# Kernel optimization log

Measured on AMD Instinct MI355X. Metric: run time of the kernel, lower is better.

The kernel has to match this reference:

```python
import jax, jax.numpy as jnp
import numpy as np

INPUT_SIZE, HIDDEN, OUTPUT = 6, 64, 3
B, T = 4096, 512


def setup_inputs() -> dict:
    key = jax.random.key(0)
    ks = jax.random.split(key, 12)
    s = 1.0 / np.sqrt(HIDDEN)  # torch LSTM/Linear default init scale
    u = lambda k, shape: jax.random.uniform(k, shape, jnp.float32, -s, s)
    return {
        "x": jax.random.normal(ks[0], (B, T, INPUT_SIZE), jnp.float32),
        "Wih0": u(ks[1], (4 * HIDDEN, INPUT_SIZE)),
        "Whh0": u(ks[2], (4 * HIDDEN, HIDDEN)),
        "bih0": u(ks[3], (4 * HIDDEN,)),
        "bhh0": u(ks[4], (4 * HIDDEN,)),
        "Wih1": u(ks[5], (4 * HIDDEN, HIDDEN)),
        "Whh1": u(ks[6], (4 * HIDDEN, HIDDEN)),
        "bih1": u(ks[7], (4 * HIDDEN,)),
        "bhh1": u(ks[8], (4 * HIDDEN,)),
        "Wfc": u(ks[9], (OUTPUT, HIDDEN)),
        "bfc": u(ks[10], (OUTPUT,)),
    }


def _lstm_layer(x, Wih, Whh, bih, bhh):
    # x: [B, T, F] -> hidden sequence [B, T, H]; torch gate order i,f,g,o
    Bn = x.shape[0]
    H = Whh.shape[1]
    b = bih + bhh
    # precompute input projections for all steps: [T, B, 4H]
    gx = jnp.einsum('btf,gf->tbg', x, Wih) + b

    def step(carry, gxt):
        h, c = carry
        gates = gxt + h @ Whh.T
        i, f, g, o = jnp.split(gates, 4, axis=-1)
        i, f, o = jax.nn.sigmoid(i), jax.nn.sigmoid(f), jax.nn.sigmoid(o)
        g = jnp.tanh(g)
        c = f * c + i * g
        h = o * jnp.tanh(c)
        return (h, c), h

    h0 = jnp.zeros((Bn, H), x.dtype)
    c0 = jnp.zeros((Bn, H), x.dtype)
    (_, _), hs = jax.lax.scan(step, (h0, c0), gx)  # hs: [T, B, H]
    return hs.transpose(1, 0, 2)


def reference(x, Wih0, Whh0, bih0, bhh0, Wih1, Whh1, bih1, bhh1, Wfc, bfc):
    h1 = _lstm_layer(x, Wih0, Whh0, bih0, bhh0)
    h2 = _lstm_layer(h1, Wih1, Whh1, bih1, bhh1)
    last = h2[:, -1, :]              # [B, H]
    return last @ Wfc.T + bfc        # [B, OUTPUT]
```

## Files before the change

kernel.cpp:

```cpp
#include <hip/hip_runtime.h>

#define H    64
#define TT   512
#define NB   16
#define OUTD 3
#define BTOT 4096
#define INF  6

typedef _Float16 f16;
typedef _Float16 f16x8 __attribute__((ext_vector_type(8)));
typedef float    f32x4 __attribute__((ext_vector_type(4)));
typedef float    f32x2 __attribute__((ext_vector_type(2)));

#define AS 168

#define LOG2E 1.44269504088896340736f
#define KSC   (2.0f * LOG2E)

static __device__ __forceinline__ f32x2 pk_fma(f32x2 a, f32x2 b, f32x2 c) {
#if __has_builtin(__builtin_elementwise_fma)
    return __builtin_elementwise_fma(a, b, c);
#else
    f32x2 r; r.x = __builtin_fmaf(a.x, b.x, c.x); r.y = __builtin_fmaf(a.y, b.y, c.y);
    return r;
#endif
}

__device__ __forceinline__ f32x2 lstm_cell2(f32x2 ai, f32x2 af, f32x2 ag, f32x2 ao,
                                            f32x2& C) {
    f32x2 ei, ef, eg, eo;
    ei.x = __builtin_amdgcn_exp2f(ai.x); ei.y = __builtin_amdgcn_exp2f(ai.y);
    ef.x = __builtin_amdgcn_exp2f(af.x); ef.y = __builtin_amdgcn_exp2f(af.y);
    eg.x = __builtin_amdgcn_exp2f(ag.x); eg.y = __builtin_amdgcn_exp2f(ag.y);
    eo.x = __builtin_amdgcn_exp2f(ao.x); eo.y = __builtin_amdgcn_exp2f(ao.y);
    f32x2 A  = ei + 1.0f;
    f32x2 F  = ef + 1.0f;
    f32x2 Bp = eg + 1.0f;
    f32x2 G  = eg - 1.0f;
    f32x2 P  = A * Bp;
    f32x2 PF = P * F;
    f32x2 r1; r1.x = __builtin_amdgcn_rcpf(PF.x); r1.y = __builtin_amdgcn_rcpf(PF.y);
    f32x2 n1 = ef * C * P;
    f32x2 t2 = ei * G * F;
    f32x2 k2 = {KSC, KSC};
    C = pk_fma(k2, t2, n1) * r1;
    f32x2 Cc; Cc.x = fminf(C.x, 126.0f); Cc.y = fminf(C.y, 126.0f);
    f32x2 ec; ec.x = __builtin_amdgcn_exp2f(Cc.x); ec.y = __builtin_amdgcn_exp2f(Cc.y);
    f32x2 D2 = (eo + 1.0f) * (ec + 1.0f);
    f32x2 r2; r2.x = __builtin_amdgcn_rcpf(D2.x); r2.y = __builtin_amdgcn_rcpf(D2.y);
    return eo * (ec - 1.0f) * r2;
}

__launch_bounds__(512, 2)
__global__ void lstm_ws(const float* __restrict__ x,
                        const float* __restrict__ Wih0, const float* __restrict__ Whh0,
                        const float* __restrict__ bih0, const float* __restrict__ bhh0,
                        const float* __restrict__ Wih1, const float* __restrict__ Whh1,
                        const float* __restrict__ bih1, const float* __restrict__ bhh1,
                        const float* __restrict__ Wfc,  const float* __restrict__ bfc,
                        float* __restrict__ out)
{
    __shared__ __align__(16) f16 Phi[2][NB * AS];
    __shared__ float hfin[NB][H + 1];

    const int t    = threadIdx.x;
    const int u    = t & 255;
    const int role = t >> 8;
    const int wv   = u >> 6;
    const int l15  = u & 15;
    const int q    = (u >> 4) & 3;
    const int jj   = 16 * wv + l15;
    const int b0   = blockIdx.x * NB;
    const int ar   = l15 * AS;
    const int ko   = q * 8;

    {
        f16* ph = &Phi[0][0];
        for (int idx = t; idx < 2 * NB * AS; idx += 512) ph[idx] = (f16)0.0f;
    }
    __syncthreads();

    const bool loader = (role == 0) && (u < NB * INF);
    const int  xb = u / INF;
    const int  xf = u - xb * INF;
    if (loader)
        Phi[0][xb * AS + 128 + xf] = (f16)x[((size_t)(b0 + xb) * TT) * INF + xf];
    __syncthreads();

    if (role == 0) {
        f16x8 wh0[2][4];
        f16x8 wx0[4];
        f32x4 bC0[4];
        #pragma unroll
        for (int g = 0; g < 4; ++g) {
            const float sc = (g == 2) ? (2.0f * LOG2E) : LOG2E;
            const int n = 64 * g + jj;
            #pragma unroll
            for (int kt = 0; kt < 2; ++kt) {
                f16x8 v;
                #pragma unroll
                for (int j = 0; j < 8; ++j)
                    v[j] = (f16)(Whh0[n * H + kt * 32 + q * 8 + j] * sc);
                wh0[kt][g] = v;
            }
            f16x8 vx;
            #pragma unroll
            for (int j = 0; j < 8; ++j)
                vx[j] = (q == 0 && j < INF) ? (f16)(Wih0[n * INF + j] * sc) : (f16)0.0f;
            wx0[g] = vx;
            const float bu = (bih0[64 * g + jj] + bhh0[64 * g + jj]) * sc;
            bC0[g] = (f32x4){bu, bu, bu, bu};
        }
        f32x2 c01 = {0.f, 0.f}, c23 = {0.f, 0.f};
        float xpre = 0.0f;

        auto stepL0 = [&](f16* __restrict__ AH, f16* __restrict__ BH, int s) {
            if (loader) {
                const int tn = (s + 1 < TT) ? (s + 1) : (TT - 1);
                xpre = x[((size_t)(b0 + xb) * TT + tn) * INF + xf];
            }
            f16x8 a0 = *(const f16x8*)&AH[ar + 0   + ko];
            f16x8 a1 = *(const f16x8*)&AH[ar + 32  + ko];
            f16x8 ax = *(const f16x8*)&BH[ar + 128 + ko];
            f32x4 accA[4];
            #pragma unroll
            for (int g = 0; g < 4; ++g) {
                f32x4 acc;
                acc = __builtin_amdgcn_mfma_f32_16x16x32_f16(a0, wh0[0][g], bC0[g], 0, 0, 0);
                acc = __builtin_amdgcn_mfma_f32_16x16x32_f16(a1, wh0[1][g], acc, 0, 0, 0);
                acc = __builtin_amdgcn_mfma_f32_16x16x32_f16(ax, wx0[g],    acc, 0, 0, 0);
                accA[g] = acc;
            }
            f32x2 h01 = lstm_cell2((f32x2){accA[0][0], accA[0][1]},
                                   (f32x2){accA[1][0], accA[1][1]},
                                   (f32x2){accA[2][0], accA[2][1]},
                                   (f32x2){accA[3][0], accA[3][1]}, c01);
            f32x2 h23 = lstm_cell2((f32x2){accA[0][2], accA[0][3]},
                                   (f32x2){accA[1][2], accA[1][3]},
                                   (f32x2){accA[2][2], accA[2][3]},
                                   (f32x2){accA[3][2], accA[3][3]}, c23);
            BH[(q * 4 + 0) * AS + jj] = (f16)h01.x;
            BH[(q * 4 + 1) * AS + jj] = (f16)h01.y;
            BH[(q * 4 + 2) * AS + jj] = (f16)h23.x;
            BH[(q * 4 + 3) * AS + jj] = (f16)h23.y;
            if (loader) AH[xb * AS + 128 + xf] = (f16)xpre;
            __syncthreads();
        };

        for (int s = 0; s < TT; s += 2) {
            stepL0(Phi[1], Phi[0], s);
            stepL0(Phi[0], Phi[1], s + 1);
        }
        __syncthreads();
    } else {
        f16x8 wi1[2][4];
        f16x8 wh1[2][4];
        f32x4 bC1[4];
        #pragma unroll
        for (int g = 0; g < 4; ++g) {
            const float sc = (g == 2) ? (2.0f * LOG2E) : LOG2E;
            const int n = 64 * g + jj;
            #pragma unroll
            for (int kt = 0; kt < 2; ++kt) {
                f16x8 v1, v2;
                #pragma unroll
                for (int j = 0; j < 8; ++j) {
                    const int k = kt * 32 + q * 8 + j;
                    v1[j] = (f16)(Wih1[n * H + k] * sc);
                    v2[j] = (f16)(Whh1[n * H + k] * sc);
                }
                wi1[kt][g] = v1; wh1[kt][g] = v2;
            }
            const float bu = (bih1[64 * g + jj] + bhh1[64 * g + jj]) * sc;
            bC1[g] = (f32x4){bu, bu, bu, bu};
        }
        f32x2 c01 = {0.f, 0.f}, c23 = {0.f, 0.f};

        __syncthreads();

        auto stepL1 = [&](f16* __restrict__ AH, f16* __restrict__ BH, int s) {
            f16x8 n0 = *(const f16x8*)&AH[ar + 0  + ko];
            f16x8 n1 = *(const f16x8*)&AH[ar + 32 + ko];
            f16x8 r0 = *(const f16x8*)&BH[ar + 64 + ko];
            f16x8 r1 = *(const f16x8*)&BH[ar + 96 + ko];
            f32x4 accB[4];
            #pragma unroll
            for (int g = 0; g < 4; ++g) {
                f32x4 acc;
                acc = __builtin_amdgcn_mfma_f32_16x16x32_f16(n0, wi1[0][g], bC1[g], 0, 0, 0);
                acc = __builtin_amdgcn_mfma_f32_16x16x32_f16(n1, wi1[1][g], acc, 0, 0, 0);
                acc = __builtin_amdgcn_mfma_f32_16x16x32_f16(r0, wh1[0][g], acc, 0, 0, 0);
                acc = __builtin_amdgcn_mfma_f32_16x16x32_f16(r1, wh1[1][g], acc, 0, 0, 0);
                accB[g] = acc;
            }
            f32x2 h01 = lstm_cell2((f32x2){accB[0][0], accB[0][1]},
                                   (f32x2){accB[1][0], accB[1][1]},
                                   (f32x2){accB[2][0], accB[2][1]},
                                   (f32x2){accB[3][0], accB[3][1]}, c01);
            f32x2 h23 = lstm_cell2((f32x2){accB[0][2], accB[0][3]},
                                   (f32x2){accB[1][2], accB[1][3]},
                                   (f32x2){accB[2][2], accB[2][3]},
                                   (f32x2){accB[3][2], accB[3][3]}, c23);
            AH[(q * 4 + 0) * AS + 64 + jj] = (f16)h01.x;
            AH[(q * 4 + 1) * AS + 64 + jj] = (f16)h01.y;
            AH[(q * 4 + 2) * AS + 64 + jj] = (f16)h23.x;
            AH[(q * 4 + 3) * AS + 64 + jj] = (f16)h23.y;
            if (s == TT) {
                hfin[q * 4 + 0][jj] = h01.x;
                hfin[q * 4 + 1][jj] = h01.y;
                hfin[q * 4 + 2][jj] = h23.x;
                hfin[q * 4 + 3][jj] = h23.y;
            }
            __syncthreads();
        };

        for (int s = 1; s <= TT; s += 2) {
            stepL1(Phi[0], Phi[1], s);
            stepL1(Phi[1], Phi[0], s + 1);
        }
    }

    if (t < NB * OUTD) {
        const int b = t / OUTD;
        const int o = t - b * OUTD;
        float a = bfc[o];
        #pragma unroll
        for (int j = 0; j < H; ++j)
            a += Wfc[o * H + j] * hfin[b][j];
        out[(size_t)(b0 + b) * OUTD + o] = a;
    }
}

extern "C" void kernel_launch(void* const* d_in, const int* in_sizes, int n_in,
                              void* d_out, int out_size, void* d_ws, size_t ws_size,
                              hipStream_t stream) {
    const float* x    = (const float*)d_in[0];
    const float* Wih0 = (const float*)d_in[1];
    const float* Whh0 = (const float*)d_in[2];
    const float* bih0 = (const float*)d_in[3];
    const float* bhh0 = (const float*)d_in[4];
    const float* Wih1 = (const float*)d_in[5];
    const float* Whh1 = (const float*)d_in[6];
    const float* bih1 = (const float*)d_in[7];
    const float* bhh1 = (const float*)d_in[8];
    const float* Wfc  = (const float*)d_in[9];
    const float* bfc  = (const float*)d_in[10];

    dim3 grid(BTOT / NB);
    dim3 block(512);
    lstm_ws<<<grid, block, 0, stream>>>(x, Wih0, Whh0, bih0, bhh0,
                                        Wih1, Whh1, bih1, bhh1,
                                        Wfc, bfc, (float*)d_out);
}
```

Before: 415.7 us.

## Duplicate each LSTM role across two wave groups and split cell math between them

```diff
diff --git a/kernel.cpp b/kernel.cpp
--- a/kernel.cpp
+++ b/kernel.cpp
@@ -22,6 +22,15 @@
     return __builtin_elementwise_fma(a, b, c);
 #else
     f32x2 r; r.x = __builtin_fmaf(a.x, b.x, c.x); r.y = __builtin_fmaf(a.y, b.y, c.y);
+    return r;
+#endif
+}
+
+static __device__ __forceinline__ f32x2 pk_min(f32x2 a, f32x2 b) {
+#if __has_builtin(__builtin_elementwise_min)
+    return __builtin_elementwise_min(a, b);
+#else
+    f32x2 r; r.x = fminf(a.x, b.x); r.y = fminf(a.y, b.y);
     return r;
 #endif
 }
@@ -44,14 +53,15 @@
     f32x2 t2 = ei * G * F;
     f32x2 k2 = {KSC, KSC};
     C = pk_fma(k2, t2, n1) * r1;
-    f32x2 Cc; Cc.x = fminf(C.x, 126.0f); Cc.y = fminf(C.y, 126.0f);
+    f32x2 clim = {126.0f, 126.0f};
+    f32x2 Cc = pk_min(C, clim);
     f32x2 ec; ec.x = __builtin_amdgcn_exp2f(Cc.x); ec.y = __builtin_amdgcn_exp2f(Cc.y);
     f32x2 D2 = (eo + 1.0f) * (ec + 1.0f);
     f32x2 r2; r2.x = __builtin_amdgcn_rcpf(D2.x); r2.y = __builtin_amdgcn_rcpf(D2.y);
     return eo * (ec - 1.0f) * r2;
 }
 
-__launch_bounds__(512, 2)
+__launch_bounds__(1024, 4)
 __global__ void lstm_ws(const float* __restrict__ x,
                         const float* __restrict__ Wih0, const float* __restrict__ Whh0,
                         const float* __restrict__ bih0, const float* __restrict__ bhh0,
@@ -65,7 +75,9 @@
 
     const int t    = threadIdx.x;
     const int u    = t & 255;
-    const int role = t >> 8;
+    const int pair = (t >> 8) & 3;
+    const int role = pair & 1;
+    const int rr   = pair >> 1;
     const int wv   = u >> 6;
     const int l15  = u & 15;
     const int q    = (u >> 4) & 3;
@@ -76,11 +88,11 @@
 
     {
         f16* ph = &Phi[0][0];
-        for (int idx = t; idx < 2 * NB * AS; idx += 512) ph[idx] = (f16)0.0f;
+        for (int idx = t; idx < 2 * NB * AS; idx += 1024) ph[idx] = (f16)0.0f;
     }
     __syncthreads();
 
-    const bool loader = (role == 0) && (u < NB * INF);
+    const bool loader = (pair == 0) && (u < NB * INF);
     const int  xb = u / INF;
     const int  xf = u - xb * INF;
     if (loader)
@@ -111,7 +123,7 @@
             const float bu = (bih0[64 * g + jj] + bhh0[64 * g + jj]) * sc;
             bC0[g] = (f32x4){bu, bu, bu, bu};
         }
-        f32x2 c01 = {0.f, 0.f}, c23 = {0.f, 0.f};
+        f32x2 c2 = {0.f, 0.f};
         float xpre = 0.0f;
 
         auto stepL0 = [&](f16* __restrict__ AH, f16* __restrict__ BH, int s) {
@@ -131,18 +143,21 @@
                 acc = __builtin_amdgcn_mfma_f32_16x16x32_f16(ax, wx0[g],    acc, 0, 0, 0);
                 accA[g] = acc;
             }
-            f32x2 h01 = lstm_cell2((f32x2){accA[0][0], accA[0][1]},
-                                   (f32x2){accA[1][0], accA[1][1]},
-                                   (f32x2){accA[2][0], accA[2][1]},
-                                   (f32x2){accA[3][0], accA[3][1]}, c01);
-            f32x2 h23 = lstm_cell2((f32x2){accA[0][2], accA[0][3]},
-                                   (f32x2){accA[1][2], accA[1][3]},
-                                   (f32x2){accA[2][2], accA[2][3]},
-                                   (f32x2){accA[3][2], accA[3][3]}, c23);
-            BH[(q * 4 + 0) * AS + jj] = (f16)h01.x;
-            BH[(q * 4 + 1) * AS + jj] = (f16)h01.y;
-            BH[(q * 4 + 2) * AS + jj] = (f16)h23.x;
-            BH[(q * 4 + 3) * AS + jj] = (f16)h23.y;
+            if (rr == 0) {
+                f32x2 hv = lstm_cell2((f32x2){accA[0][0], accA[0][1]},
+                                      (f32x2){accA[1][0], accA[1][1]},
+                                      (f32x2){accA[2][0], accA[2][1]},
+                                      (f32x2){accA[3][0], accA[3][1]}, c2);
+                BH[(q * 4 + 0) * AS + jj] = (f16)hv.x;
+                BH[(q * 4 + 1) * AS + jj] = (f16)hv.y;
+            } else {
+                f32x2 hv = lstm_cell2((f32x2){accA[0][2], accA[0][3]},
+                                      (f32x2){accA[1][2], accA[1][3]},
+                                      (f32x2){accA[2][2], accA[2][3]},
+                                      (f32x2){accA[3][2], accA[3][3]}, c2);
+                BH[(q * 4 + 2) * AS + jj] = (f16)hv.x;
+                BH[(q * 4 + 3) * AS + jj] = (f16)hv.y;
+            }
             if (loader) AH[xb * AS + 128 + xf] = (f16)xpre;
             __syncthreads();
         };
@@ -174,7 +189,7 @@
             const float bu = (bih1[64 * g + jj] + bhh1[64 * g + jj]) * sc;
             bC1[g] = (f32x4){bu, bu, bu, bu};
         }
-        f32x2 c01 = {0.f, 0.f}, c23 = {0.f, 0.f};
+        f32x2 c2 = {0.f, 0.f};
 
         __syncthreads();
 
@@ -193,23 +208,28 @@
                 acc = __builtin_amdgcn_mfma_f32_16x16x32_f16(r1, wh1[1][g], acc, 0, 0, 0);
                 accB[g] = acc;
             }
-            f32x2 h01 = lstm_cell2((f32x2){accB[0][0], accB[0][1]},
-                                   (f32x2){accB[1][0], accB[1][1]},
-                                   (f32x2){accB[2][0], accB[2][1]},
-                                   (f32x2){accB[3][0], accB[3][1]}, c01);
-            f32x2 h23 = lstm_cell2((f32x2){accB[0][2], accB[0][3]},
-                                   (f32x2){accB[1][2], accB[1][3]},
-                                   (f32x2){accB[2][2], accB[2][3]},
-                                   (f32x2){accB[3][2], accB[3][3]}, c23);
-            AH[(q * 4 + 0) * AS + 64 + jj] = (f16)h01.x;
-            AH[(q * 4 + 1) * AS + 64 + jj] = (f16)h01.y;
-            AH[(q * 4 + 2) * AS + 64 + jj] = (f16)h23.x;
-            AH[(q * 4 + 3) * AS + 64 + jj] = (f16)h23.y;
-            if (s == TT) {
-                hfin[q * 4 + 0][jj] = h01.x;
-                hfin[q * 4 + 1][jj] = h01.y;
-                hfin[q * 4 + 2][jj] = h23.x;
-                hfin[q * 4 + 3][jj] = h23.y;
+            if (rr == 0) {
+                f32x2 hv = lstm_cell2((f32x2){accB[0][0], accB[0][1]},
+                                      (f32x2){accB[1][0], accB[1][1]},
+                                      (f32x2){accB[2][0], accB[2][1]},
+                                      (f32x2){accB[3][0], accB[3][1]}, c2);
+                AH[(q * 4 + 0) * AS + 64 + jj] = (f16)hv.x;
+                AH[(q * 4 + 1) * AS + 64 + jj] = (f16)hv.y;
+                if (s == TT) {
+                    hfin[q * 4 + 0][jj] = hv.x;
+                    hfin[q * 4 + 1][jj] = hv.y;
+                }
+            } else {
+                f32x2 hv = lstm_cell2((f32x2){accB[0][2], accB[0][3]},
+                                      (f32x2){accB[1][2], accB[1][3]},
+                                      (f32x2){accB[2][2], accB[2][3]},
+                                      (f32x2){accB[3][2], accB[3][3]}, c2);
+                AH[(q * 4 + 2) * AS + 64 + jj] = (f16)hv.x;
+                AH[(q * 4 + 3) * AS + 64 + jj] = (f16)hv.y;
+                if (s == TT) {
+                    hfin[q * 4 + 2][jj] = hv.x;
+                    hfin[q * 4 + 3][jj] = hv.y;
+                }
             }
             __syncthreads();
         };
@@ -247,7 +267,7 @@
     const float* bfc  = (const float*)d_in[10];
 
     dim3 grid(BTOT / NB);
-    dim3 block(512);
+    dim3 block(1024);
     lstm_ws<<<grid, block, 0, stream>>>(x, Wih0, Whh0, bih0, bhh0,
                                         Wih1, Whh1, bih1, bhh1,
                                         Wfc, bfc, (float*)d_out);
```

Measured after the change: 519.7 us. +25.0%, slower.

## Replace block barriers with LDS flag counters and 4-deep ring buffers between layers

Applied to the files above, without the earlier changes.

```diff
diff --git a/kernel.cpp b/kernel.cpp
--- a/kernel.cpp
+++ b/kernel.cpp
@@ -6,13 +6,14 @@
 #define OUTD 3
 #define BTOT 4096
 #define INF  6
+#define RD   4
+#define HS   72
+#define XS   32
 
 typedef _Float16 f16;
 typedef _Float16 f16x8 __attribute__((ext_vector_type(8)));
 typedef float    f32x4 __attribute__((ext_vector_type(4)));
 typedef float    f32x2 __attribute__((ext_vector_type(2)));
-
-#define AS 168
 
 #define LOG2E 1.44269504088896340736f
 #define KSC   (2.0f * LOG2E)
@@ -22,6 +23,15 @@
     return __builtin_elementwise_fma(a, b, c);
 #else
     f32x2 r; r.x = __builtin_fmaf(a.x, b.x, c.x); r.y = __builtin_fmaf(a.y, b.y, c.y);
+    return r;
+#endif
+}
+
+static __device__ __forceinline__ f32x2 pk_min(f32x2 a, f32x2 b) {
+#if __has_builtin(__builtin_elementwise_min)
+    return __builtin_elementwise_min(a, b);
+#else
+    f32x2 r; r.x = fminf(a.x, b.x); r.y = fminf(a.y, b.y);
     return r;
 #endif
 }
@@ -44,11 +54,23 @@
     f32x2 t2 = ei * G * F;
     f32x2 k2 = {KSC, KSC};
     C = pk_fma(k2, t2, n1) * r1;
-    f32x2 Cc; Cc.x = fminf(C.x, 126.0f); Cc.y = fminf(C.y, 126.0f);
+    f32x2 clim = {126.0f, 126.0f};
+    f32x2 Cc = pk_min(C, clim);
     f32x2 ec; ec.x = __builtin_amdgcn_exp2f(Cc.x); ec.y = __builtin_amdgcn_exp2f(Cc.y);
     f32x2 D2 = (eo + 1.0f) * (ec + 1.0f);
     f32x2 r2; r2.x = __builtin_amdgcn_rcpf(D2.x); r2.y = __builtin_amdgcn_rcpf(D2.y);
     return eo * (ec - 1.0f) * r2;
+}
+
+static __device__ __forceinline__ void wait_ge(const unsigned* p, unsigned tgt) {
+    volatile const unsigned* vp = (volatile const unsigned*)p;
+    while (*vp < tgt) {}
+    asm volatile("" ::: "memory");
+}
+
+static __device__ __forceinline__ void bump(unsigned* p, bool lane0) {
+    asm volatile("s_waitcnt lgkmcnt(0)" ::: "memory");
+    if (lane0) atomicAdd(p, 1u);
 }
 
 __launch_bounds__(512, 2)
@@ -60,31 +82,35 @@
                         const float* __restrict__ Wfc,  const float* __restrict__ bfc,
                         float* __restrict__ out)
 {
-    __shared__ __align__(16) f16 Phi[2][NB * AS];
+    __shared__ __align__(16) f16 H0r[RD][NB * HS];
+    __shared__ __align__(16) f16 H1r[RD][NB * HS];
+    __shared__ __align__(16) f16 Xr[RD][NB * XS];
     __shared__ float hfin[NB][H + 1];
-
-    const int t    = threadIdx.x;
-    const int u    = t & 255;
-    const int role = t >> 8;
-    const int wv   = u >> 6;
-    const int l15  = u & 15;
-    const int q    = (u >> 4) & 3;
-    const int jj   = 16 * wv + l15;
-    const int b0   = blockIdx.x * NB;
-    const int ar   = l15 * AS;
-    const int ko   = q * 8;
-
-    {
-        f16* ph = &Phi[0][0];
-        for (int idx = t; idx < 2 * NB * AS; idx += 512) ph[idx] = (f16)0.0f;
-    }
+    __shared__ unsigned flg[12];
+
+    const int t     = threadIdx.x;
+    const int u     = t & 255;
+    const int role  = t >> 8;
+    const int wv    = u >> 6;
+    const int l15   = u & 15;
+    const int q     = (u >> 4) & 3;
+    const int jj    = 16 * wv + l15;
+    const int b0    = blockIdx.x * NB;
+    const int ar    = l15 * HS;
+    const int ko    = q * 8;
+    const bool lane0 = (t & 63) == 0;
+
+    for (int idx = t; idx < RD * NB * HS; idx += 512) (&H0r[0][0])[idx] = (f16)0.0f;
+    for (int idx = t; idx < RD * NB * HS; idx += 512) (&H1r[0][0])[idx] = (f16)0.0f;
+    for (int idx = t; idx < RD * NB * XS; idx += 512) (&Xr[0][0])[idx]  = (f16)0.0f;
+    if (t < 12) flg[t] = 0u;
     __syncthreads();
 
     const bool loader = (role == 0) && (u < NB * INF);
     const int  xb = u / INF;
     const int  xf = u - xb * INF;
     if (loader)
-        Phi[0][xb * AS + 128 + xf] = (f16)x[((size_t)(b0 + xb) * TT) * INF + xf];
+        Xr[0][xb * XS + xf] = (f16)x[((size_t)(b0 + xb) * TT) * INF + xf];
     __syncthreads();
 
     if (role == 0) {
@@ -114,14 +140,20 @@
         f32x2 c01 = {0.f, 0.f}, c23 = {0.f, 0.f};
         float xpre = 0.0f;
 
-        auto stepL0 = [&](f16* __restrict__ AH, f16* __restrict__ BH, int s) {
+        #pragma unroll 4
+        for (int s = 0; s < TT; ++s) {
+            const int j  = s & 3;
+            const int jp = (s - 1) & 3;
+            const int jn = (s + 1) & 3;
+            if (s > 0) wait_ge(&flg[jp], 4u * (unsigned)((s - 1) >> 2) + 4u);
             if (loader) {
                 const int tn = (s + 1 < TT) ? (s + 1) : (TT - 1);
                 xpre = x[((size_t)(b0 + xb) * TT + tn) * INF + xf];
             }
-            f16x8 a0 = *(const f16x8*)&AH[ar + 0   + ko];
-            f16x8 a1 = *(const f16x8*)&AH[ar + 32  + ko];
-            f16x8 ax = *(const f16x8*)&BH[ar + 128 + ko];
+            const f16* Ah = &H0r[jp][0];
+            f16x8 a0 = *(const f16x8*)&Ah[ar + 0  + ko];
+            f16x8 a1 = *(const f16x8*)&Ah[ar + 32 + ko];
+            f16x8 ax = *(const f16x8*)&Xr[j][l15 * XS + ko];
             f32x4 accA[4];
             #pragma unroll
             for (int g = 0; g < 4; ++g) {
@@ -139,19 +171,15 @@
                                    (f32x2){accA[1][2], accA[1][3]},
                                    (f32x2){accA[2][2], accA[2][3]},
                                    (f32x2){accA[3][2], accA[3][3]}, c23);
-            BH[(q * 4 + 0) * AS + jj] = (f16)h01.x;
-            BH[(q * 4 + 1) * AS + jj] = (f16)h01.y;
-            BH[(q * 4 + 2) * AS + jj] = (f16)h23.x;
-            BH[(q * 4 + 3) * AS + jj] = (f16)h23.y;
-            if (loader) AH[xb * AS + 128 + xf] = (f16)xpre;
-            __syncthreads();
-        };
-
-        for (int s = 0; s < TT; s += 2) {
-            stepL0(Phi[1], Phi[0], s);
-            stepL0(Phi[0], Phi[1], s + 1);
-        }
-        __syncthreads();
+            if (s >= RD) wait_ge(&flg[8 + j], 4u * (unsigned)(s >> 2));
+            f16* Bh = &H0r[j][0];
+            Bh[(q * 4 + 0) * HS + jj] = (f16)h01.x;
+            Bh[(q * 4 + 1) * HS + jj] = (f16)h01.y;
+            Bh[(q * 4 + 2) * HS + jj] = (f16)h23.x;
+            Bh[(q * 4 + 3) * HS + jj] = (f16)h23.y;
+            if (loader) Xr[jn][xb * XS + xf] = (f16)xpre;
+            bump(&flg[j], lane0);
+        }
     } else {
         f16x8 wi1[2][4];
         f16x8 wh1[2][4];
@@ -176,13 +204,19 @@
         }
         f32x2 c01 = {0.f, 0.f}, c23 = {0.f, 0.f};
 
-        __syncthreads();
-
-        auto stepL1 = [&](f16* __restrict__ AH, f16* __restrict__ BH, int s) {
-            f16x8 n0 = *(const f16x8*)&AH[ar + 0  + ko];
-            f16x8 n1 = *(const f16x8*)&AH[ar + 32 + ko];
-            f16x8 r0 = *(const f16x8*)&BH[ar + 64 + ko];
-            f16x8 r1 = *(const f16x8*)&BH[ar + 96 + ko];
+        #pragma unroll 4
+        for (int m = 0; m < TT; ++m) {
+            const int j  = m & 3;
+            const int jp = (m - 1) & 3;
+            wait_ge(&flg[j], 4u * (unsigned)(m >> 2) + 4u);
+            if (m > 0) wait_ge(&flg[4 + jp], 4u * (unsigned)((m - 1) >> 2) + 4u);
+            const f16* Nh = &H0r[j][0];
+            const f16* Rh = &H1r[jp][0];
+            f16x8 n0 = *(const f16x8*)&Nh[ar + 0  + ko];
+            f16x8 n1 = *(const f16x8*)&Nh[ar + 32 + ko];
+            f16x8 r0 = *(const f16x8*)&Rh[ar + 0  + ko];
+            f16x8 r1 = *(const f16x8*)&Rh[ar + 32 + ko];
+            bump(&flg[8 + j], lane0);
             f32x4 accB[4];
             #pragma unroll
             for (int g = 0; g < 4; ++g) {
@@ -199,26 +233,24 @@
                                    (f32x2){accB[3][0], accB[3][1]}, c01);
             f32x2 h23 = lstm_cell2((f32x2){accB[0][2], accB[0][3]},
                                    (f32x2){accB[1][2], accB[1][3]},
-                                   (f32x2){accB[2][2], accB[2][3]},
+                                   (f32x2){accB[2][2], accB[2][3]}, 
                                    (f32x2){accB[3][2], accB[3][3]}, c23);
-            AH[(q * 4 + 0) * AS + 64 + jj] = (f16)h01.x;
-            AH[(q * 4 + 1) * AS + 64 + jj] = (f16)h01.y;
-            AH[(q * 4 + 2) * AS + 64 + jj] = (f16)h23.x;
-            AH[(q * 4 + 3) * AS + 64 + jj] = (f16)h23.y;
-            if (s == TT) {
+            f16* Wh = &H1r[j][0];
+            Wh[(q * 4 + 0) * HS + jj] = (f16)h01.x;
+            Wh[(q * 4 + 1) * HS + jj] = (f16)h01.y;
+            Wh[(q * 4 + 2) * HS + jj] = (f16)h23.x;
+            Wh[(q * 4 + 3) * HS + jj] = (f16)h23.y;
+            if (m == TT - 1) {
                 hfin[q * 4 + 0][jj] = h01.x;
                 hfin[q * 4 + 1][jj] = h01.y;
                 hfin[q * 4 + 2][jj] = h23.x;
                 hfin[q * 4 + 3][jj] = h23.y;
             }
-            __syncthreads();
-        };
-
-        for (int s = 1; s <= TT; s += 2) {
-            stepL1(Phi[0], Phi[1], s);
-            stepL1(Phi[1], Phi[0], s + 1);
+            bump(&flg[4 + j], lane0);
         }
     }
+
+    __syncthreads();
 
     if (t < NB * OUTD) {
         const int b = t / OUTD;
```

Measured after the change: 494.8 us. 1.19x slower.

## Fuse both LSTM layers into a single 256-thread wavefront schedule per block

Applied to the files above, without the earlier changes.

```diff
diff --git a/kernel.cpp b/kernel.cpp
--- a/kernel.cpp
+++ b/kernel.cpp
@@ -6,13 +6,13 @@
 #define OUTD 3
 #define BTOT 4096
 #define INF  6
+#define HS   72
+#define XS   32
 
 typedef _Float16 f16;
 typedef _Float16 f16x8 __attribute__((ext_vector_type(8)));
 typedef float    f32x4 __attribute__((ext_vector_type(4)));
 typedef float    f32x2 __attribute__((ext_vector_type(2)));
-
-#define AS 168
 
 #define LOG2E 1.44269504088896340736f
 #define KSC   (2.0f * LOG2E)
@@ -22,6 +22,15 @@
     return __builtin_elementwise_fma(a, b, c);
 #else
     f32x2 r; r.x = __builtin_fmaf(a.x, b.x, c.x); r.y = __builtin_fmaf(a.y, b.y, c.y);
+    return r;
+#endif
+}
+
+static __device__ __forceinline__ f32x2 pk_min(f32x2 a, f32x2 b) {
+#if __has_builtin(__builtin_elementwise_min)
+    return __builtin_elementwise_min(a, b);
+#else
+    f32x2 r; r.x = fminf(a.x, b.x); r.y = fminf(a.y, b.y);
     return r;
 #endif
 }
@@ -44,180 +53,175 @@
     f32x2 t2 = ei * G * F;
     f32x2 k2 = {KSC, KSC};
     C = pk_fma(k2, t2, n1) * r1;
-    f32x2 Cc; Cc.x = fminf(C.x, 126.0f); Cc.y = fminf(C.y, 126.0f);
+    f32x2 clim = {126.0f, 126.0f};
+    f32x2 Cc = pk_min(C, clim);
     f32x2 ec; ec.x = __builtin_amdgcn_exp2f(Cc.x); ec.y = __builtin_amdgcn_exp2f(Cc.y);
     f32x2 D2 = (eo + 1.0f) * (ec + 1.0f);
     f32x2 r2; r2.x = __builtin_amdgcn_rcpf(D2.x); r2.y = __builtin_amdgcn_rcpf(D2.y);
     return eo * (ec - 1.0f) * r2;
 }
 
-__launch_bounds__(512, 2)
-__global__ void lstm_ws(const float* __restrict__ x,
-                        const float* __restrict__ Wih0, const float* __restrict__ Whh0,
-                        const float* __restrict__ bih0, const float* __restrict__ bhh0,
-                        const float* __restrict__ Wih1, const float* __restrict__ Whh1,
-                        const float* __restrict__ bih1, const float* __restrict__ bhh1,
-                        const float* __restrict__ Wfc,  const float* __restrict__ bfc,
-                        float* __restrict__ out)
+__launch_bounds__(256, 1)
+__global__ void lstm_fused(const float* __restrict__ x,
+                           const float* __restrict__ Wih0, const float* __restrict__ Whh0,
+                           const float* __restrict__ bih0, const float* __restrict__ bhh0,
+                           const float* __restrict__ Wih1, const float* __restrict__ Whh1,
+                           const float* __restrict__ bih1, const float* __restrict__ bhh1,
+                           const float* __restrict__ Wfc,  const float* __restrict__ bfc,
+                           float* __restrict__ out)
 {
-    __shared__ __align__(16) f16 Phi[2][NB * AS];
+    __shared__ __align__(16) f16 H0[2][NB * HS];
+    __shared__ __align__(16) f16 H1[2][NB * HS];
+    __shared__ __align__(16) f16 Xr[2][NB * XS];
     __shared__ float hfin[NB][H + 1];
 
-    const int t    = threadIdx.x;
-    const int u    = t & 255;
-    const int role = t >> 8;
-    const int wv   = u >> 6;
-    const int l15  = u & 15;
-    const int q    = (u >> 4) & 3;
-    const int jj   = 16 * wv + l15;
-    const int b0   = blockIdx.x * NB;
-    const int ar   = l15 * AS;
-    const int ko   = q * 8;
+    const int t   = threadIdx.x;
+    const int wv  = t >> 6;
+    const int l15 = t & 15;
+    const int q   = (t >> 4) & 3;
+    const int jj  = 16 * wv + l15;
+    const int b0  = blockIdx.x * NB;
+    const int ar  = l15 * HS;
+    const int ko  = q * 8;
+
+    for (int idx = t; idx < 2 * NB * HS; idx += 256) {
+        (&H0[0][0])[idx] = (f16)0.0f;
+        (&H1[0][0])[idx] = (f16)0.0f;
+    }
+    for (int idx = t; idx < 2 * NB * XS; idx += 256) (&Xr[0][0])[idx] = (f16)0.0f;
+    __syncthreads();
+
+    const bool loader = t < NB * INF;
+    const int  xb = t / INF;
+    const int  xf = t - xb * INF;
+    if (loader)
+        Xr[0][xb * XS + xf] = (f16)x[((size_t)(b0 + xb) * TT) * INF + xf];
+
+    f16x8 wh0[2][4], wx0[4], wi1[2][4], wh1[2][4];
+    f32x4 bC0[4], bC1[4];
+    #pragma unroll
+    for (int g = 0; g < 4; ++g) {
+        const float sc = (g == 2) ? KSC : LOG2E;
+        const int n = 64 * g + jj;
+        #pragma unroll
+        for (int kt = 0; kt < 2; ++kt) {
+            f16x8 v0, v1, v2;
+            #pragma unroll
+            for (int j = 0; j < 8; ++j) {
+                const int k = kt * 32 + q * 8 + j;
+                v0[j] = (f16)(Whh0[n * H + k] * sc);
+                v1[j] = (f16)(Wih1[n * H + k] * sc);
+                v2[j] = (f16)(Whh1[n * H + k] * sc);
+            }
+            wh0[kt][g] = v0; wi1[kt][g] = v1; wh1[kt][g] = v2;
+        }
+        f16x8 vx;
+        #pragma unroll
+        for (int j = 0; j < 8; ++j)
+            vx[j] = (q == 0 && j < INF) ? (f16)(Wih0[n * INF + j] * sc) : (f16)0.0f;
+        wx0[g] = vx;
+        const float bu0 = (bih0[64 * g + jj] + bhh0[64 * g + jj]) * sc;
+        const float bu1 = (bih1[64 * g + jj] + bhh1[64 * g + jj]) * sc;
+        bC0[g] = (f32x4){bu0, bu0, bu0, bu0};
+        bC1[g] = (f32x4){bu1, bu1, bu1, bu1};
+    }
+    f32x2 c0a = {0.f, 0.f}, c0b = {0.f, 0.f};
+    f32x2 c1a = {0.f, 0.f}, c1b = {0.f, 0.f};
+    float xpre = 0.0f;
+    __syncthreads();
+
+    auto mfmaA = [&](f16x8 a0, f16x8 a1, f16x8 ax, f32x4* acc) {
+        #pragma unroll
+        for (int g = 0; g < 4; ++g) {
+            f32x4 a = __builtin_amdgcn_mfma_f32_16x16x32_f16(a0, wh0[0][g], bC0[g], 0, 0, 0);
+            a = __builtin_amdgcn_mfma_f32_16x16x32_f16(a1, wh0[1][g], a, 0, 0, 0);
+            a = __builtin_amdgcn_mfma_f32_16x16x32_f16(ax, wx0[g],    a, 0, 0, 0);
+            acc[g] = a;
+        }
+    };
+    auto mfmaB = [&](f16x8 a0, f16x8 a1, f16x8 r0, f16x8 r1, f32x4* acc) {
+        #pragma unroll
+        for (int g = 0; g < 4; ++g) {
+            f32x4 a = __builtin_amdgcn_mfma_f32_16x16x32_f16(a0, wi1[0][g], bC1[g], 0, 0, 0);
+            a = __builtin_amdgcn_mfma_f32_16x16x32_f16(a1, wi1[1][g], a, 0, 0, 0);
+            a = __builtin_amdgcn_mfma_f32_16x16x32_f16(r0, wh1[0][g], a, 0, 0, 0);
+            a = __builtin_amdgcn_mfma_f32_16x16x32_f16(r1, wh1[1][g], a, 0, 0, 0);
+            acc[g] = a;
+        }
+    };
+    auto cellWrite = [&](f32x4* acc, f32x2& ca, f32x2& cb, f16* dst) {
+        f32x2 h01 = lstm_cell2((f32x2){acc[0][0], acc[0][1]},
+                               (f32x2){acc[1][0], acc[1][1]},
+                               (f32x2){acc[2][0], acc[2][1]},
+                               (f32x2){acc[3][0], acc[3][1]}, ca);
+        f32x2 h23 = lstm_cell2((f32x2){acc[0][2], acc[0][3]},
+                               (f32x2){acc[1][2], acc[1][3]},
+                               (f32x2){acc[2][2], acc[2][3]}, 
+                               (f32x2){acc[3][2], acc[3][3]}, cb);
+        dst[(q * 4 + 0) * HS + jj] = (f16)h01.x;
+        dst[(q * 4 + 1) * HS + jj] = (f16)h01.y;
+        dst[(q * 4 + 2) * HS + jj] = (f16)h23.x;
+        dst[(q * 4 + 3) * HS + jj] = (f16)h23.y;
+    };
 
     {
-        f16* ph = &Phi[0][0];
-        for (int idx = t; idx < 2 * NB * AS; idx += 512) ph[idx] = (f16)0.0f;
-    }
-    __syncthreads();
-
-    const bool loader = (role == 0) && (u < NB * INF);
-    const int  xb = u / INF;
-    const int  xf = u - xb * INF;
-    if (loader)
-        Phi[0][xb * AS + 128 + xf] = (f16)x[((size_t)(b0 + xb) * TT) * INF + xf];
-    __syncthreads();
-
-    if (role == 0) {
-        f16x8 wh0[2][4];
-        f16x8 wx0[4];
-        f32x4 bC0[4];
-        #pragma unroll
-        for (int g = 0; g < 4; ++g) {
-            const float sc = (g == 2) ? (2.0f * LOG2E) : LOG2E;
-            const int n = 64 * g + jj;
-            #pragma unroll
-            for (int kt = 0; kt < 2; ++kt) {
-                f16x8 v;
-                #pragma unroll
-                for (int j = 0; j < 8; ++j)
-                    v[j] = (f16)(Whh0[n * H + kt * 32 + q * 8 + j] * sc);
-                wh0[kt][g] = v;
-            }
-            f16x8 vx;
-            #pragma unroll
-            for (int j = 0; j < 8; ++j)
-                vx[j] = (q == 0 && j < INF) ? (f16)(Wih0[n * INF + j] * sc) : (f16)0.0f;
-            wx0[g] = vx;
-            const float bu = (bih0[64 * g + jj] + bhh0[64 * g + jj]) * sc;
-            bC0[g] = (f32x4){bu, bu, bu, bu};
-        }
-        f32x2 c01 = {0.f, 0.f}, c23 = {0.f, 0.f};
-        float xpre = 0.0f;
-
-        auto stepL0 = [&](f16* __restrict__ AH, f16* __restrict__ BH, int s) {
-            if (loader) {
-                const int tn = (s + 1 < TT) ? (s + 1) : (TT - 1);
-                xpre = x[((size_t)(b0 + xb) * TT + tn) * INF + xf];
-            }
-            f16x8 a0 = *(const f16x8*)&AH[ar + 0   + ko];
-            f16x8 a1 = *(const f16x8*)&AH[ar + 32  + ko];
-            f16x8 ax = *(const f16x8*)&BH[ar + 128 + ko];
-            f32x4 accA[4];
-            #pragma unroll
-            for (int g = 0; g < 4; ++g) {
-                f32x4 acc;
-                acc = __builtin_amdgcn_mfma_f32_16x16x32_f16(a0, wh0[0][g], bC0[g], 0, 0, 0);
-                acc = __builtin_amdgcn_mfma_f32_16x16x32_f16(a1, wh0[1][g], acc, 0, 0, 0);
-                acc = __builtin_amdgcn_mfma_f32_16x16x32_f16(ax, wx0[g],    acc, 0, 0, 0);
-                accA[g] = acc;
-            }
-            f32x2 h01 = lstm_cell2((f32x2){accA[0][0], accA[0][1]},
-                                   (f32x2){accA[1][0], accA[1][1]},
-                                   (f32x2){accA[2][0], accA[2][1]},
-                                   (f32x2){accA[3][0], accA[3][1]}, c01);
-            f32x2 h23 = lstm_cell2((f32x2){accA[0][2], accA[0][3]},
-                                   (f32x2){accA[1][2], accA[1][3]},
-                                   (f32x2){accA[2][2], accA[2][3]},
-                                   (f32x2){accA[3][2], accA[3][3]}, c23);
-            BH[(q * 4 + 0) * AS + jj] = (f16)h01.x;
-            BH[(q * 4 + 1) * AS + jj] = (f16)h01.y;
-            BH[(q * 4 + 2) * AS + jj] = (f16)h23.x;
-            BH[(q * 4 + 3) * AS + jj] = (f16)h23.y;
-            if (loader) AH[xb * AS + 128 + xf] = (f16)xpre;
-            __syncthreads();
-        };
-
-        for (int s = 0; s < TT; s += 2) {
-            stepL0(Phi[1], Phi[0], s);
-            stepL0(Phi[0], Phi[1], s + 1);
-        }
+        if (loader) xpre = x[((size_t)(b0 + xb) * TT + 1) * INF + xf];
+        const f16* h0r = &H0[1][0];
+        f16x8 a0 = *(const f16x8*)&h0r[ar + ko];
+        f16x8 a1 = *(const f16x8*)&h0r[ar + 32 + ko];
+        f16x8 ax = *(const f16x8*)&Xr[0][l15 * XS + ko];
+        f32x4 accA[4];
+        mfmaA(a0, a1, ax, accA);
+        cellWrite(accA, c0a, c0b, &H0[0][0]);
+        if (loader) Xr[1][xb * XS + xf] = (f16)xpre;
         __syncthreads();
-    } else {
-        f16x8 wi1[2][4];
-        f16x8 wh1[2][4];
-        f32x4 bC1[4];
-        #pragma unroll
-        for (int g = 0; g < 4; ++g) {
-            const float sc = (g == 2) ? (2.0f * LOG2E) : LOG2E;
-            const int n = 64 * g + jj;
-            #pragma unroll
-            for (int kt = 0; kt < 2; ++kt) {
-                f16x8 v1, v2;
-                #pragma unroll
-                for (int j = 0; j < 8; ++j) {
-                    const int k = kt * 32 + q * 8 + j;
-                    v1[j] = (f16)(Wih1[n * H + k] * sc);
-                    v2[j] = (f16)(Whh1[n * H + k] * sc);
-                }
-                wi1[kt][g] = v1; wh1[kt][g] = v2;
-            }
-            const float bu = (bih1[64 * g + jj] + bhh1[64 * g + jj]) * sc;
-            bC1[g] = (f32x4){bu, bu, bu, bu};
-        }
-        f32x2 c01 = {0.f, 0.f}, c23 = {0.f, 0.f};
-
+    }
+
+    #pragma unroll 2
+    for (int s = 1; s < TT; ++s) {
+        const int p = s & 1, pp = p ^ 1;
+        if (loader) {
+            const int tn = (s + 1 < TT) ? (s + 1) : (TT - 1);
+            xpre = x[((size_t)(b0 + xb) * TT + tn) * INF + xf];
+        }
+        const f16* h0r = &H0[pp][0];
+        const f16* h1r = &H1[p][0];
+        f16x8 a0 = *(const f16x8*)&h0r[ar + ko];
+        f16x8 a1 = *(const f16x8*)&h0r[ar + 32 + ko];
+        f16x8 ax = *(const f16x8*)&Xr[p][l15 * XS + ko];
+        f16x8 r0 = *(const f16x8*)&h1r[ar + ko];
+        f16x8 r1 = *(const f16x8*)&h1r[ar + 32 + ko];
+        f32x4 accA[4], accB[4];
+        mfmaA(a0, a1, ax, accA);
+        mfmaB(a0, a1, r0, r1, accB);
+        cellWrite(accA, c0a, c0b, &H0[p][0]);
+        cellWrite(accB, c1a, c1b, &H1[pp][0]);
+        if (loader) Xr[pp][xb * XS + xf] = (f16)xpre;
         __syncthreads();
-
-        auto stepL1 = [&](f16* __restrict__ AH, f16* __restrict__ BH, int s) {
-            f16x8 n0 = *(const f16x8*)&AH[ar + 0  + ko];
-            f16x8 n1 = *(const f16x8*)&AH[ar + 32 + ko];
-            f16x8 r0 = *(const f16x8*)&BH[ar + 64 + ko];
-            f16x8 r1 = *(const f16x8*)&BH[ar + 96 + ko];
-            f32x4 accB[4];
-            #pragma unroll
-            for (int g = 0; g < 4; ++g) {
-                f32x4 acc;
-                acc = __builtin_amdgcn_mfma_f32_16x16x32_f16(n0, wi1[0][g], bC1[g], 0, 0, 0);
-                acc = __builtin_amdgcn_mfma_f32_16x16x32_f16(n1, wi1[1][g], acc, 0, 0, 0);
-                acc = __builtin_amdgcn_mfma_f32_16x16x32_f16(r0, wh1[0][g], acc, 0, 0, 0);
-                acc = __builtin_amdgcn_mfma_f32_16x16x32_f16(r1, wh1[1][g], acc, 0, 0, 0);
-                accB[g] = acc;
-            }
-            f32x2 h01 = lstm_cell2((f32x2){accB[0][0], accB[0][1]},
-                                   (f32x2){accB[1][0], accB[1][1]},
-                                   (f32x2){accB[2][0], accB[2][1]},
-                                   (f32x2){accB[3][0], accB[3][1]}, c01);
-            f32x2 h23 = lstm_cell2((f32x2){accB[0][2], accB[0][3]},
-                                   (f32x2){accB[1][2], accB[1][3]},
-                                   (f32x2){accB[2][2], accB[2][3]},
-                                   (f32x2){accB[3][2], accB[3][3]}, c23);
-            AH[(q * 4 + 0) * AS + 64 + jj] = (f16)h01.x;
-            AH[(q * 4 + 1) * AS + 64 + jj] = (f16)h01.y;
-            AH[(q * 4 + 2) * AS + 64 + jj] = (f16)h23.x;
-            AH[(q * 4 + 3) * AS + 64 + jj] = (f16)h23.y;
-            if (s == TT) {
-                hfin[q * 4 + 0][jj] = h01.x;
-                hfin[q * 4 + 1][jj] = h01.y;
-                hfin[q * 4 + 2][jj] = h23.x;
-                hfin[q * 4 + 3][jj] = h23.y;
-            }
-            __syncthreads();
-        };
-
-        for (int s = 1; s <= TT; s += 2) {
-            stepL1(Phi[0], Phi[1], s);
-            stepL1(Phi[1], Phi[0], s + 1);
-        }
+    }
+
+    {
+        const f16* h0r = &H0[1][0];
+        const f16* h1r = &H1[0][0];
+        f16x8 a0 = *(const f16x8*)&h0r[ar + ko];
+        f16x8 a1 = *(const f16x8*)&h0r[ar + 32 + ko];
+        f16x8 r0 = *(const f16x8*)&h1r[ar + ko];
+        f16x8 r1 = *(const f16x8*)&h1r[ar + 32 + ko];
+        f32x4 accB[4];
+        mfmaB(a0, a1, r0, r1, accB);
+        f32x2 h01 = lstm_cell2((f32x2){accB[0][0], accB[0][1]},
+                               (f32x2){accB[1][0], accB[1][1]},
+                               (f32x2){accB[2][0], accB[2][1]},
+                               (f32x2){accB[3][0], accB[3][1]}, c1a);
+        f32x2 h23 = lstm_cell2((f32x2){accB[0][2], accB[0][3]},
+                               (f32x2){accB[1][2], accB[1][3]},
+                               (f32x2){accB[2][2], accB[2][3]},
+                               (f32x2){accB[3][2], accB[3][3]}, c1b);
+        hfin[q * 4 + 0][jj] = h01.x;
+        hfin[q * 4 + 1][jj] = h01.y;
+        hfin[q * 4 + 2][jj] = h23.x;
+        hfin[q * 4 + 3][jj] = h23.y;
+        __syncthreads();
     }
 
     if (t < NB * OUTD) {
@@ -247,8 +251,8 @@
     const float* bfc  = (const float*)d_in[10];
 
     dim3 grid(BTOT / NB);
-    dim3 block(512);
-    lstm_ws<<<grid, block, 0, stream>>>(x, Wih0, Whh0, bih0, bhh0,
-                                        Wih1, Whh1, bih1, bhh1,
-                                        Wfc, bfc, (float*)d_out);
-}
+    dim3 block(256);
+    lstm_fused<<<grid, block, 0, stream>>>(x, Wih0, Whh0, bih0, bhh0,
+                                           Wih1, Whh1, bih1, bhh1,
+                                           Wfc, bfc, (float*)d_out);
+}
```

Measured after the change: 469.6 us. +13.0%, slower.
